# Performance work log

Hardware: AMD Instinct MI355X
Metric: run time of the kernel (lower is better)

Reference implementation:

```python
import math
import jax, jax.numpy as jnp
import numpy as np

B, T, C = 2, 2048, 1024
N_HEAD, N_KV_HEAD = 16, 4
HEAD_DIM = C // N_HEAD  # 64

def _rope(x, cos, sin):
    # x: (B, T, H, D); cos/sin: (1, T, 1, D//2)
    d = x.shape[3] // 2
    x1, x2 = x[..., :d], x[..., d:]
    return jnp.concatenate([x1 * cos + x2 * sin, -x1 * sin + x2 * cos], axis=3)

def _rms_norm(x):
    return x * jax.lax.rsqrt(jnp.mean(x * x, axis=-1, keepdims=True) + 1e-06)

def setup_inputs() -> dict:
    key = jax.random.key(0)
    ks = jax.random.split(key, 9)
    x = jax.random.normal(ks[0], (B, T, C), dtype=jnp.float32)
    ve = jax.random.normal(ks[1], (B, T, N_KV_HEAD * HEAD_DIM), dtype=jnp.float32)
    cos = jax.random.uniform(ks[2], (1, T, 1, HEAD_DIM // 2), dtype=jnp.float32)
    sin = jax.random.uniform(ks[3], (1, T, 1, HEAD_DIM // 2), dtype=jnp.float32)
    s = 1.0 / math.sqrt(C)
    Wq = jax.random.normal(ks[4], (C, N_HEAD * HEAD_DIM), dtype=jnp.float32) * s
    Wk = jax.random.normal(ks[5], (C, N_KV_HEAD * HEAD_DIM), dtype=jnp.float32) * s
    Wv = jax.random.normal(ks[6], (C, N_KV_HEAD * HEAD_DIM), dtype=jnp.float32) * s
    Wproj = jax.random.normal(ks[7], (C, C), dtype=jnp.float32) * s
    Wg = jax.random.normal(ks[8], (12, N_KV_HEAD), dtype=jnp.float32) * (1.0 / math.sqrt(12))
    return {"x": x, "ve": ve, "cos": cos, "sin": sin,
            "Wq": Wq, "Wk": Wk, "Wv": Wv, "Wproj": Wproj, "Wg": Wg,
            "window_size": 1024}

def reference(x, ve, cos, sin, Wq, Wk, Wv, Wproj, Wg, window_size):
    Bb, Tt, Cc = x.shape
    q = (x @ Wq).reshape(Bb, Tt, N_HEAD, HEAD_DIM)
    k = (x @ Wk).reshape(Bb, Tt, N_KV_HEAD, HEAD_DIM)
    v = (x @ Wv).reshape(Bb, Tt, N_KV_HEAD, HEAD_DIM)
    # value-embedding gate (has_ve layer)
    vee = ve.reshape(Bb, Tt, N_KV_HEAD, HEAD_DIM)
    gate = 3.0 * jax.nn.sigmoid(x[..., :12] @ Wg)  # (B, T, n_kv_head)
    v = v + gate[..., None] * vee
    q = _rope(q, cos, sin)
    k = _rope(k, cos, sin)
    q = _rms_norm(q) * 1.2
    k = _rms_norm(k) * 1.2
    repeats = N_HEAD // N_KV_HEAD
    k = jnp.repeat(k, repeats, axis=2)
    v = jnp.repeat(v, repeats, axis=2)
    # sliding-window causal mask
    row = jnp.arange(Tt)[:, None]
    col = jnp.arange(Tt)[None, :]
    mask = (row >= col) & (row - col <= window_size)
    bias = jnp.where(mask, 0.0, -1e9)  # (T, T)
    scale = 1.0 / math.sqrt(HEAD_DIM)
    scores = jnp.einsum("bqhd,bkhd->bhqk", q, k) * scale + bias[None, None]
    attn = jax.nn.softmax(scores, axis=-1)
    y = jnp.einsum("bhqk,bkhd->bqhd", attn, v).reshape(Bb, Tt, Cc)
    return y @ Wproj
```

## Files before the change

### kernel.cpp

```cpp
#include <hip/hip_runtime.h>


typedef __bf16 bf16x8 __attribute__((ext_vector_type(8)));
typedef __bf16 bf16x4 __attribute__((ext_vector_type(4)));
typedef float  f32x4  __attribute__((ext_vector_type(4)));

__device__ __forceinline__ void g2l16(const __bf16* gp, __bf16* lp) {
  __builtin_amdgcn_global_load_lds(
      (const __attribute__((address_space(1))) unsigned int*)(const void*)gp,
      (__attribute__((address_space(3))) unsigned int*)(void*)lp, 16, 0, 0);
}

__global__ void convert_gate(const float* __restrict__ in, __bf16* __restrict__ out,
                             float* __restrict__ gate, const float* __restrict__ Wg) {
  int i = (blockIdx.x * blockDim.x + threadIdx.x) * 8;
  float4 a = *(const float4*)(in + i);
  float4 b = *(const float4*)(in + i + 4);
  bf16x8 o;
  o[0] = (__bf16)a.x; o[1] = (__bf16)a.y; o[2] = (__bf16)a.z; o[3] = (__bf16)a.w;
  o[4] = (__bf16)b.x; o[5] = (__bf16)b.y; o[6] = (__bf16)b.z; o[7] = (__bf16)b.w;
  *(bf16x8*)(out + i) = o;
  if (threadIdx.x < 8) {
    int row = blockIdx.x * 2 + (threadIdx.x >> 2);
    int kvh = threadIdx.x & 3;
    float dot = 0.f;
    for (int j = 0; j < 12; ++j) dot += in[(size_t)row * 1024 + j] * Wg[j * 4 + kvh];
    gate[row * 4 + kvh] = 3.f / (1.f + expf(-dot));
  }
}

__global__ void transpose_weights(const float* __restrict__ Wq, const float* __restrict__ Wk,
                                  const float* __restrict__ Wv, const float* __restrict__ Wp,
                                  __bf16* __restrict__ Wt, __bf16* __restrict__ Wpt) {
  __shared__ float tile[32][33];
  int z = blockIdx.z;
  const float* in; __bf16* out; int Cc;
  if (z == 0)      { in = Wq; out = Wt;                 Cc = 1024; }
  else if (z == 1) { in = Wk; out = Wt + 1024 * 1024;   Cc = 256; }
  else if (z == 2) { in = Wv; out = Wt + 1280 * 1024;   Cc = 256; }
  else             { in = Wp; out = Wpt;                Cc = 1024; }
  const int R = 1024;
  int c0 = blockIdx.x * 32, r0 = blockIdx.y * 32;
  if (c0 >= Cc) return;
  int tx = threadIdx.x & 31, ty = threadIdx.x >> 5;
  for (int i = ty; i < 32; i += 8) tile[i][tx] = in[(size_t)(r0 + i) * Cc + c0 + tx];
  __syncthreads();
  for (int i = ty; i < 32; i += 8) out[(size_t)(c0 + i) * R + r0 + tx] = (__bf16)tile[tx][i];
}

__global__ __launch_bounds__(256) void gemm_qkv(const __bf16* __restrict__ A,
                                                const __bf16* __restrict__ Bt,
                                                const float* __restrict__ cosp,
                                                const float* __restrict__ sinp,
                                                const float* __restrict__ gate,
                                                const float* __restrict__ ve,
                                                __bf16* __restrict__ Qb,
                                                __bf16* __restrict__ Kb,
                                                __bf16* __restrict__ Vt) {
  const int K = 1024;
  __shared__ __bf16 As[128 * 32];
  __shared__ __bf16 Bs[128 * 32];
  int tid = threadIdx.x;
  int m0 = blockIdx.y * 128, n0 = blockIdx.x * 128;
  int w = tid >> 6, lane = tid & 63, quad = lane >> 4, l16 = lane & 15;
  int wm = (w >> 1) * 64, wn = (w & 1) * 64;

  f32x4 zero = {0.f, 0.f, 0.f, 0.f};
  f32x4 acc[4][4];
  for (int i = 0; i < 4; ++i) for (int j = 0; j < 4; ++j) acc[i][j] = zero;

  int ch0 = w * 2, ch1 = w * 2 + 1;
  int rsub = lane >> 2, cc = (lane & 3) * 8;
  const __bf16* gA0 = A + (size_t)(m0 + ch0 * 16 + rsub) * K + cc;
  const __bf16* gA1 = A + (size_t)(m0 + ch1 * 16 + rsub) * K + cc;
  const __bf16* gB0 = Bt + (size_t)(n0 + ch0 * 16 + rsub) * K + cc;
  const __bf16* gB1 = Bt + (size_t)(n0 + ch1 * 16 + rsub) * K + cc;
  __bf16* lA0 = &As[ch0 * 512]; __bf16* lA1 = &As[ch1 * 512];
  __bf16* lB0 = &Bs[ch0 * 512]; __bf16* lB1 = &Bs[ch1 * 512];

  for (int k0 = 0; k0 < K; k0 += 32) {
    __syncthreads();
    g2l16(gA0 + k0, lA0);
    g2l16(gA1 + k0, lA1);
    g2l16(gB0 + k0, lB0);
    g2l16(gB1 + k0, lB1);
    __syncthreads();
    bf16x8 af[4], bfr[4];
    for (int i = 0; i < 4; ++i) {
      af[i]  = *(const bf16x8*)(&As[(wm + i * 16 + l16) * 32 + quad * 8]);
      bfr[i] = *(const bf16x8*)(&Bs[(wn + i * 16 + l16) * 32 + quad * 8]);
    }
    for (int i = 0; i < 4; ++i)
      for (int j = 0; j < 4; ++j)
        acc[i][j] = __builtin_amdgcn_mfma_f32_16x16x32_bf16(af[i], bfr[j], acc[i][j], 0, 0, 0);
  }

  int ncol = n0 + wn;
  if (ncol < 1280) {
    __bf16* dstbase;
    if (ncol < 1024) dstbase = Qb + (size_t)(ncol >> 6) * 2048 * 64;
    else             dstbase = Kb + (size_t)((ncol - 1024) >> 6) * 2048 * 64;
    int nheads = (ncol < 1024) ? 16 : 4;
    for (int i = 0; i < 4; ++i) {
      for (int r = 0; r < 4; ++r) {
        int m = m0 + wm + i * 16 + quad * 4 + r;
        int bb = m >> 11, t = m & 2047;
        float c0 = cosp[t * 32 + l16], c1 = cosp[t * 32 + 16 + l16];
        float s0 = sinp[t * 32 + l16], s1 = sinp[t * 32 + 16 + l16];
        float v0 = acc[i][0][r], v1 = acc[i][1][r], v2 = acc[i][2][r], v3 = acc[i][3][r];
        float r0 = v0 * c0 + v2 * s0;
        float r1 = v1 * c1 + v3 * s1;
        float r2 = v2 * c0 - v0 * s0;
        float r3 = v3 * c1 - v1 * s1;
        float ss = r0 * r0 + r1 * r1 + r2 * r2 + r3 * r3;
        ss += __shfl_xor(ss, 1, 64); ss += __shfl_xor(ss, 2, 64);
        ss += __shfl_xor(ss, 4, 64); ss += __shfl_xor(ss, 8, 64);
        float sc = rsqrtf(ss * (1.f / 64.f) + 1e-6f) * 1.2f;
        __bf16* dst = dstbase + ((size_t)bb * nheads * 2048 + t) * 64;
        dst[l16]      = (__bf16)(r0 * sc);
        dst[16 + l16] = (__bf16)(r1 * sc);
        dst[32 + l16] = (__bf16)(r2 * sc);
        dst[48 + l16] = (__bf16)(r3 * sc);
      }
    }
  } else {
    int kvh = (ncol - 1280) >> 6;
    for (int i = 0; i < 4; ++i) {
      int mbase = m0 + wm + i * 16 + quad * 4;
      int bb = mbase >> 11;
      int t0 = mbase & 2047;
      float g4[4];
      for (int r = 0; r < 4; ++r) g4[r] = gate[(mbase + r) * 4 + kvh];
      for (int j = 0; j < 4; ++j) {
        int d = j * 16 + l16;
        bf16x4 pk;
        for (int r = 0; r < 4; ++r)
          pk[r] = (__bf16)(acc[i][j][r] + g4[r] * ve[(size_t)(mbase + r) * 256 + kvh * 64 + d]);
        *(bf16x4*)(Vt + ((size_t)(bb * 4 + kvh) * 64 + d) * 2048 + t0) = pk;
      }
    }
  }
}

__global__ __launch_bounds__(512) void attn_kernel(
    const __bf16* __restrict__ Q, const __bf16* __restrict__ K,
    const __bf16* __restrict__ Vt, __bf16* __restrict__ Y,
    const int* __restrict__ winp) {
  const int T = 2048, D = 64, NH = 16, NKV = 4;
  int b = blockIdx.z, h = blockIdx.y;
  int qb = (15 - blockIdx.x) * 128;
  int kvh = h >> 2;
  int tid = threadIdx.x, w = tid >> 6, lane = tid & 63, quad = lane >> 4, l16 = lane & 15;
  int window = *winp;
  int qw = qb + w * 16;

  __shared__ __bf16 Ks[64 * 72];
  __shared__ __bf16 Vs[64 * 72];
  __shared__ __bf16 Ps[8 * 16 * 72];

  const __bf16* Qbase = Q + ((size_t)(b * NH + h)) * T * D;
  bf16x8 qf0 = *(const bf16x8*)(Qbase + (size_t)(qw + l16) * D + quad * 8);
  bf16x8 qf1 = *(const bf16x8*)(Qbase + (size_t)(qw + l16) * D + quad * 8 + 32);

  const __bf16* Kbase = K  + ((size_t)(b * NKV + kvh)) * T * D;
  const __bf16* Vbase = Vt + ((size_t)(b * NKV + kvh)) * D * T;

  float lsum[4] = {0.f, 0.f, 0.f, 0.f};
  f32x4 zero = {0.f, 0.f, 0.f, 0.f};
  f32x4 o[4] = {zero, zero, zero, zero};

  int kstart = qb - window; if (kstart < 0) kstart = 0; kstart &= ~63;
  int kend = qb + 128;
  const float c1 = 0.125f * 1.44269504f;
  const float c2 = 12.0f * 1.44269504f;

  int sr = tid >> 3, sc8 = (tid & 7) * 8;
  bf16x8 kr = *(const bf16x8*)(Kbase + (size_t)(kstart + sr) * D + sc8);
  bf16x8 vr = *(const bf16x8*)(Vbase + (size_t)sr * T + kstart + sc8);

  for (int kt = kstart; kt < kend; kt += 64) {
    __syncthreads();
    *(bf16x8*)(&Ks[sr * 72 + sc8]) = kr;
    *(bf16x8*)(&Vs[sr * 72 + sc8]) = vr;
    __syncthreads();
    int ktn = kt + 64;
    if (ktn < kend) {
      kr = *(const bf16x8*)(Kbase + (size_t)(ktn + sr) * D + sc8);
      vr = *(const bf16x8*)(Vbase + (size_t)sr * T + ktn + sc8);
    }
    if (kt > qw + 15 || kt + 63 < qw - window) continue;

    f32x4 s[4];
    for (int kg = 0; kg < 4; ++kg) {
      bf16x8 k0 = *(const bf16x8*)(&Ks[(kg * 16 + l16) * 72 + quad * 8]);
      bf16x8 k1 = *(const bf16x8*)(&Ks[(kg * 16 + l16) * 72 + quad * 8 + 32]);
      s[kg] = __builtin_amdgcn_mfma_f32_16x16x32_bf16(qf0, k0, zero, 0, 0, 0);
      s[kg] = __builtin_amdgcn_mfma_f32_16x16x32_bf16(qf1, k1, s[kg], 0, 0, 0);
    }
    for (int r = 0; r < 4; ++r) {
      int q = qw + quad * 4 + r;
      for (int kg = 0; kg < 4; ++kg) {
        int ki = kt + kg * 16 + l16;
        bool ok = (ki <= q) && (q - ki <= window);
        float p = ok ? exp2f(s[kg][r] * c1 - c2) : 0.f;
        lsum[r] += p;
        Ps[w * 1152 + (quad * 4 + r) * 72 + kg * 16 + l16] = (__bf16)p;
      }
    }
    for (int koff = 0; koff < 64; koff += 32) {
      bf16x8 pf = *(const bf16x8*)(&Ps[w * 1152 + l16 * 72 + koff + quad * 8]);
      for (int j = 0; j < 4; ++j) {
        bf16x8 vf = *(const bf16x8*)(&Vs[(j * 16 + l16) * 72 + koff + quad * 8]);
        o[j] = __builtin_amdgcn_mfma_f32_16x16x32_bf16(pf, vf, o[j], 0, 0, 0);
      }
    }
  }

  for (int r = 0; r < 4; ++r) {
    float l = lsum[r];
    for (int off = 1; off < 16; off <<= 1) l += __shfl_xor(l, off, 64);
    float inv = 1.f / l;
    size_t base = ((size_t)(b * T + qw + quad * 4 + r)) * 1024 + h * 64 + l16;
    Y[base +  0] = (__bf16)(o[0][r] * inv);
    Y[base + 16] = (__bf16)(o[1][r] * inv);
    Y[base + 32] = (__bf16)(o[2][r] * inv);
    Y[base + 48] = (__bf16)(o[3][r] * inv);
  }
}

__global__ __launch_bounds__(256) void gemm_bt(const __bf16* __restrict__ A,
                                               const __bf16* __restrict__ Bt,
                                               float* __restrict__ C,
                                               int M, int N, int K) {
  __shared__ __bf16 As[128 * 32];
  __shared__ __bf16 Bs[128 * 32];
  int tid = threadIdx.x;
  int m0 = blockIdx.y * 128, n0 = blockIdx.x * 128;
  int w = tid >> 6, lane = tid & 63, quad = lane >> 4, l16 = lane & 15;
  int wm = (w >> 1) * 64, wn = (w & 1) * 64;

  f32x4 zero = {0.f, 0.f, 0.f, 0.f};
  f32x4 acc[4][4];
  for (int i = 0; i < 4; ++i) for (int j = 0; j < 4; ++j) acc[i][j] = zero;

  int ch0 = w * 2, ch1 = w * 2 + 1;
  int rsub = lane >> 2, cc = (lane & 3) * 8;
  const __bf16* gA0 = A + (size_t)(m0 + ch0 * 16 + rsub) * K + cc;
  const __bf16* gA1 = A + (size_t)(m0 + ch1 * 16 + rsub) * K + cc;
  const __bf16* gB0 = Bt + (size_t)(n0 + ch0 * 16 + rsub) * K + cc;
  const __bf16* gB1 = Bt + (size_t)(n0 + ch1 * 16 + rsub) * K + cc;
  __bf16* lA0 = &As[ch0 * 512]; __bf16* lA1 = &As[ch1 * 512];
  __bf16* lB0 = &Bs[ch0 * 512]; __bf16* lB1 = &Bs[ch1 * 512];

  for (int k0 = 0; k0 < K; k0 += 32) {
    __syncthreads();
    g2l16(gA0 + k0, lA0);
    g2l16(gA1 + k0, lA1);
    g2l16(gB0 + k0, lB0);
    g2l16(gB1 + k0, lB1);
    __syncthreads();
    bf16x8 af[4], bfr[4];
    for (int i = 0; i < 4; ++i) {
      af[i]  = *(const bf16x8*)(&As[(wm + i * 16 + l16) * 32 + quad * 8]);
      bfr[i] = *(const bf16x8*)(&Bs[(wn + i * 16 + l16) * 32 + quad * 8]);
    }
    for (int i = 0; i < 4; ++i)
      for (int j = 0; j < 4; ++j)
        acc[i][j] = __builtin_amdgcn_mfma_f32_16x16x32_bf16(af[i], bfr[j], acc[i][j], 0, 0, 0);
  }
  for (int i = 0; i < 4; ++i)
    for (int j = 0; j < 4; ++j)
      for (int r = 0; r < 4; ++r)
        C[(size_t)(m0 + wm + i * 16 + quad * 4 + r) * N + n0 + wn + j * 16 + l16] = acc[i][j][r];
}

extern "C" void kernel_launch(void* const* d_in, const int* in_sizes, int n_in,
                              void* d_out, int out_size, void* d_ws, size_t ws_size,
                              hipStream_t stream) {
  const float* x     = (const float*)d_in[0];
  const float* ve    = (const float*)d_in[1];
  const float* cosp  = (const float*)d_in[2];
  const float* sinp  = (const float*)d_in[3];
  const float* Wq    = (const float*)d_in[4];
  const float* Wk    = (const float*)d_in[5];
  const float* Wv    = (const float*)d_in[6];
  const float* Wproj = (const float*)d_in[7];
  const float* Wg    = (const float*)d_in[8];
  const int*   win   = (const int*)d_in[9];
  float* out = (float*)d_out;

  char* ws = (char*)d_ws;
  __bf16* xb   = (__bf16*)(ws);
  __bf16* Wt   = (__bf16*)(ws + 8388608);
  __bf16* Wpt  = (__bf16*)(ws + 11534336);
  float*  gate = (float*)(ws + 13631488);
  __bf16* Qb   = (__bf16*)(ws + 13697024);
  __bf16* Kb   = (__bf16*)(ws + 22085632);
  __bf16* Vt   = (__bf16*)(ws + 24182784);
  __bf16* Y    = (__bf16*)(ws + 26279936);

  convert_gate<<<2048, 256, 0, stream>>>(x, xb, gate, Wg);
  transpose_weights<<<dim3(32, 32, 4), 256, 0, stream>>>(Wq, Wk, Wv, Wproj, Wt, Wpt);
  gemm_qkv<<<dim3(12, 32), 256, 0, stream>>>(xb, Wt, cosp, sinp, gate, ve, Qb, Kb, Vt);
  attn_kernel<<<dim3(16, 16, 2), 512, 0, stream>>>(Qb, Kb, Vt, Y, win);
  gemm_bt<<<dim3(8, 32), 256, 0, stream>>>(Y, Wpt, out, 4096, 1024, 1024);
}
```

Before: 198.5 us.

## Merge prep kernels, halve GEMM M-tiles, restructure attention to direct global K/V loads

```diff
diff --git a/kernel.cpp b/kernel.cpp
--- a/kernel.cpp
+++ b/kernel.cpp
@@ -11,41 +11,44 @@
       (__attribute__((address_space(3))) unsigned int*)(void*)lp, 16, 0, 0);
 }
 
-__global__ void convert_gate(const float* __restrict__ in, __bf16* __restrict__ out,
-                             float* __restrict__ gate, const float* __restrict__ Wg) {
-  int i = (blockIdx.x * blockDim.x + threadIdx.x) * 8;
-  float4 a = *(const float4*)(in + i);
-  float4 b = *(const float4*)(in + i + 4);
-  bf16x8 o;
-  o[0] = (__bf16)a.x; o[1] = (__bf16)a.y; o[2] = (__bf16)a.z; o[3] = (__bf16)a.w;
-  o[4] = (__bf16)b.x; o[5] = (__bf16)b.y; o[6] = (__bf16)b.z; o[7] = (__bf16)b.w;
-  *(bf16x8*)(out + i) = o;
-  if (threadIdx.x < 8) {
-    int row = blockIdx.x * 2 + (threadIdx.x >> 2);
-    int kvh = threadIdx.x & 3;
-    float dot = 0.f;
-    for (int j = 0; j < 12; ++j) dot += in[(size_t)row * 1024 + j] * Wg[j * 4 + kvh];
-    gate[row * 4 + kvh] = 3.f / (1.f + expf(-dot));
-  }
-}
-
-__global__ void transpose_weights(const float* __restrict__ Wq, const float* __restrict__ Wk,
-                                  const float* __restrict__ Wv, const float* __restrict__ Wp,
-                                  __bf16* __restrict__ Wt, __bf16* __restrict__ Wpt) {
+__global__ void prep(const float* __restrict__ x, __bf16* __restrict__ xb,
+                     float* __restrict__ gate, const float* __restrict__ Wg,
+                     const float* __restrict__ Wq, const float* __restrict__ Wk,
+                     const float* __restrict__ Wv, const float* __restrict__ Wp,
+                     __bf16* __restrict__ Wt, __bf16* __restrict__ Wpt) {
   __shared__ float tile[32][33];
-  int z = blockIdx.z;
+  int bid = blockIdx.x;
+  if (bid < 2048) {
+    int i = (bid * 256 + threadIdx.x) * 8;
+    float4 a = *(const float4*)(x + i);
+    float4 b = *(const float4*)(x + i + 4);
+    bf16x8 o;
+    o[0] = (__bf16)a.x; o[1] = (__bf16)a.y; o[2] = (__bf16)a.z; o[3] = (__bf16)a.w;
+    o[4] = (__bf16)b.x; o[5] = (__bf16)b.y; o[6] = (__bf16)b.z; o[7] = (__bf16)b.w;
+    *(bf16x8*)(xb + i) = o;
+    if (threadIdx.x < 8) {
+      int row = bid * 2 + (threadIdx.x >> 2);
+      int kvh = threadIdx.x & 3;
+      float dot = 0.f;
+      for (int j = 0; j < 12; ++j) dot += x[(size_t)row * 1024 + j] * Wg[j * 4 + kvh];
+      gate[row * 4 + kvh] = 3.f / (1.f + expf(-dot));
+    }
+    return;
+  }
+  bid -= 2048;
+  int z = bid >> 10, r = bid & 1023;
+  int bx = r & 31, by = r >> 5;
   const float* in; __bf16* out; int Cc;
-  if (z == 0)      { in = Wq; out = Wt;                 Cc = 1024; }
-  else if (z == 1) { in = Wk; out = Wt + 1024 * 1024;   Cc = 256; }
-  else if (z == 2) { in = Wv; out = Wt + 1280 * 1024;   Cc = 256; }
-  else             { in = Wp; out = Wpt;                Cc = 1024; }
-  const int R = 1024;
-  int c0 = blockIdx.x * 32, r0 = blockIdx.y * 32;
+  if (z == 0)      { in = Wq; out = Wt;               Cc = 1024; }
+  else if (z == 1) { in = Wk; out = Wt + 1024 * 1024; Cc = 256; }
+  else if (z == 2) { in = Wv; out = Wt + 1280 * 1024; Cc = 256; }
+  else             { in = Wp; out = Wpt;              Cc = 1024; }
+  int c0 = bx * 32, r0 = by * 32;
   if (c0 >= Cc) return;
   int tx = threadIdx.x & 31, ty = threadIdx.x >> 5;
   for (int i = ty; i < 32; i += 8) tile[i][tx] = in[(size_t)(r0 + i) * Cc + c0 + tx];
   __syncthreads();
-  for (int i = ty; i < 32; i += 8) out[(size_t)(c0 + i) * R + r0 + tx] = (__bf16)tile[tx][i];
+  for (int i = ty; i < 32; i += 8) out[(size_t)(c0 + i) * 1024 + r0 + tx] = (__bf16)tile[tx][i];
 }
 
 __global__ __launch_bounds__(256) void gemm_qkv(const __bf16* __restrict__ A,
@@ -58,39 +61,37 @@
                                                 __bf16* __restrict__ Kb,
                                                 __bf16* __restrict__ Vt) {
   const int K = 1024;
-  __shared__ __bf16 As[128 * 32];
+  __shared__ __bf16 As[64 * 32];
   __shared__ __bf16 Bs[128 * 32];
   int tid = threadIdx.x;
-  int m0 = blockIdx.y * 128, n0 = blockIdx.x * 128;
+  int m0 = blockIdx.y * 64, n0 = blockIdx.x * 128;
   int w = tid >> 6, lane = tid & 63, quad = lane >> 4, l16 = lane & 15;
-  int wm = (w >> 1) * 64, wn = (w & 1) * 64;
+  int wm = (w >> 1) * 32, wn = (w & 1) * 64;
 
   f32x4 zero = {0.f, 0.f, 0.f, 0.f};
-  f32x4 acc[4][4];
-  for (int i = 0; i < 4; ++i) for (int j = 0; j < 4; ++j) acc[i][j] = zero;
-
-  int ch0 = w * 2, ch1 = w * 2 + 1;
+  f32x4 acc[2][4];
+  for (int i = 0; i < 2; ++i) for (int j = 0; j < 4; ++j) acc[i][j] = zero;
+
   int rsub = lane >> 2, cc = (lane & 3) * 8;
-  const __bf16* gA0 = A + (size_t)(m0 + ch0 * 16 + rsub) * K + cc;
-  const __bf16* gA1 = A + (size_t)(m0 + ch1 * 16 + rsub) * K + cc;
-  const __bf16* gB0 = Bt + (size_t)(n0 + ch0 * 16 + rsub) * K + cc;
-  const __bf16* gB1 = Bt + (size_t)(n0 + ch1 * 16 + rsub) * K + cc;
-  __bf16* lA0 = &As[ch0 * 512]; __bf16* lA1 = &As[ch1 * 512];
-  __bf16* lB0 = &Bs[ch0 * 512]; __bf16* lB1 = &Bs[ch1 * 512];
+  const __bf16* gA  = A  + (size_t)(m0 + w * 16 + rsub) * K + cc;
+  const __bf16* gB0 = Bt + (size_t)(n0 + (2 * w) * 16 + rsub) * K + cc;
+  const __bf16* gB1 = Bt + (size_t)(n0 + (2 * w + 1) * 16 + rsub) * K + cc;
+  __bf16* lA  = &As[w * 512];
+  __bf16* lB0 = &Bs[(2 * w) * 512];
+  __bf16* lB1 = &Bs[(2 * w + 1) * 512];
 
   for (int k0 = 0; k0 < K; k0 += 32) {
     __syncthreads();
-    g2l16(gA0 + k0, lA0);
-    g2l16(gA1 + k0, lA1);
+    g2l16(gA + k0, lA);
     g2l16(gB0 + k0, lB0);
     g2l16(gB1 + k0, lB1);
     __syncthreads();
-    bf16x8 af[4], bfr[4];
-    for (int i = 0; i < 4; ++i) {
-      af[i]  = *(const bf16x8*)(&As[(wm + i * 16 + l16) * 32 + quad * 8]);
-      bfr[i] = *(const bf16x8*)(&Bs[(wn + i * 16 + l16) * 32 + quad * 8]);
-    }
-    for (int i = 0; i < 4; ++i)
+    bf16x8 af[2], bfr[4];
+    for (int i = 0; i < 2; ++i)
+      af[i] = *(const bf16x8*)(&As[(wm + i * 16 + l16) * 32 + quad * 8]);
+    for (int j = 0; j < 4; ++j)
+      bfr[j] = *(const bf16x8*)(&Bs[(wn + j * 16 + l16) * 32 + quad * 8]);
+    for (int i = 0; i < 2; ++i)
       for (int j = 0; j < 4; ++j)
         acc[i][j] = __builtin_amdgcn_mfma_f32_16x16x32_bf16(af[i], bfr[j], acc[i][j], 0, 0, 0);
   }
@@ -101,7 +102,7 @@
     if (ncol < 1024) dstbase = Qb + (size_t)(ncol >> 6) * 2048 * 64;
     else             dstbase = Kb + (size_t)((ncol - 1024) >> 6) * 2048 * 64;
     int nheads = (ncol < 1024) ? 16 : 4;
-    for (int i = 0; i < 4; ++i) {
+    for (int i = 0; i < 2; ++i) {
       for (int r = 0; r < 4; ++r) {
         int m = m0 + wm + i * 16 + quad * 4 + r;
         int bb = m >> 11, t = m & 2047;
@@ -125,7 +126,7 @@
     }
   } else {
     int kvh = (ncol - 1280) >> 6;
-    for (int i = 0; i < 4; ++i) {
+    for (int i = 0; i < 2; ++i) {
       int mbase = m0 + wm + i * 16 + quad * 4;
       int bb = mbase >> 11;
       int t0 = mbase & 2047;
@@ -142,21 +143,19 @@
   }
 }
 
-__global__ __launch_bounds__(512) void attn_kernel(
+__global__ __launch_bounds__(256) void attn_kernel(
     const __bf16* __restrict__ Q, const __bf16* __restrict__ K,
     const __bf16* __restrict__ Vt, __bf16* __restrict__ Y,
     const int* __restrict__ winp) {
   const int T = 2048, D = 64, NH = 16, NKV = 4;
   int b = blockIdx.z, h = blockIdx.y;
-  int qb = (15 - blockIdx.x) * 128;
+  int qb = (31 - blockIdx.x) * 64;
   int kvh = h >> 2;
   int tid = threadIdx.x, w = tid >> 6, lane = tid & 63, quad = lane >> 4, l16 = lane & 15;
   int window = *winp;
   int qw = qb + w * 16;
 
-  __shared__ __bf16 Ks[64 * 72];
-  __shared__ __bf16 Vs[64 * 72];
-  __shared__ __bf16 Ps[8 * 16 * 72];
+  __shared__ __bf16 Ps[4 * 16 * 72];
 
   const __bf16* Qbase = Q + ((size_t)(b * NH + h)) * T * D;
   bf16x8 qf0 = *(const bf16x8*)(Qbase + (size_t)(qw + l16) * D + quad * 8);
@@ -169,50 +168,54 @@
   f32x4 zero = {0.f, 0.f, 0.f, 0.f};
   f32x4 o[4] = {zero, zero, zero, zero};
 
-  int kstart = qb - window; if (kstart < 0) kstart = 0; kstart &= ~63;
-  int kend = qb + 128;
+  int kw = qw - window;
+  int kt0 = (kw > 0) ? (kw & ~63) : 0;
+  int ktlast = (qw + 15) & ~63;
   const float c1 = 0.125f * 1.44269504f;
   const float c2 = 12.0f * 1.44269504f;
 
-  int sr = tid >> 3, sc8 = (tid & 7) * 8;
-  bf16x8 kr = *(const bf16x8*)(Kbase + (size_t)(kstart + sr) * D + sc8);
-  bf16x8 vr = *(const bf16x8*)(Vbase + (size_t)sr * T + kstart + sc8);
-
-  for (int kt = kstart; kt < kend; kt += 64) {
-    __syncthreads();
-    *(bf16x8*)(&Ks[sr * 72 + sc8]) = kr;
-    *(bf16x8*)(&Vs[sr * 72 + sc8]) = vr;
-    __syncthreads();
-    int ktn = kt + 64;
-    if (ktn < kend) {
-      kr = *(const bf16x8*)(Kbase + (size_t)(ktn + sr) * D + sc8);
-      vr = *(const bf16x8*)(Vbase + (size_t)sr * T + ktn + sc8);
-    }
-    if (kt > qw + 15 || kt + 63 < qw - window) continue;
-
+  for (int kt = kt0; kt <= ktlast; kt += 64) {
+    bf16x8 kf0[4], kf1[4];
+    for (int kg = 0; kg < 4; ++kg) {
+      const __bf16* gK = Kbase + (size_t)(kt + kg * 16 + l16) * D + quad * 8;
+      kf0[kg] = *(const bf16x8*)(gK);
+      kf1[kg] = *(const bf16x8*)(gK + 32);
+    }
+    bf16x8 vf[2][4];
+    for (int j = 0; j < 4; ++j) {
+      const __bf16* gV = Vbase + (size_t)(j * 16 + l16) * T + kt + quad * 8;
+      vf[0][j] = *(const bf16x8*)(gV);
+      vf[1][j] = *(const bf16x8*)(gV + 32);
+    }
     f32x4 s[4];
     for (int kg = 0; kg < 4; ++kg) {
-      bf16x8 k0 = *(const bf16x8*)(&Ks[(kg * 16 + l16) * 72 + quad * 8]);
-      bf16x8 k1 = *(const bf16x8*)(&Ks[(kg * 16 + l16) * 72 + quad * 8 + 32]);
-      s[kg] = __builtin_amdgcn_mfma_f32_16x16x32_bf16(qf0, k0, zero, 0, 0, 0);
-      s[kg] = __builtin_amdgcn_mfma_f32_16x16x32_bf16(qf1, k1, s[kg], 0, 0, 0);
-    }
-    for (int r = 0; r < 4; ++r) {
-      int q = qw + quad * 4 + r;
-      for (int kg = 0; kg < 4; ++kg) {
-        int ki = kt + kg * 16 + l16;
-        bool ok = (ki <= q) && (q - ki <= window);
-        float p = ok ? exp2f(s[kg][r] * c1 - c2) : 0.f;
-        lsum[r] += p;
-        Ps[w * 1152 + (quad * 4 + r) * 72 + kg * 16 + l16] = (__bf16)p;
+      s[kg] = __builtin_amdgcn_mfma_f32_16x16x32_bf16(qf0, kf0[kg], zero, 0, 0, 0);
+      s[kg] = __builtin_amdgcn_mfma_f32_16x16x32_bf16(qf1, kf1[kg], s[kg], 0, 0, 0);
+    }
+    bool clean = (kt + 63 <= qw) && (qw + 15 - kt <= window);
+    if (clean) {
+      for (int r = 0; r < 4; ++r)
+        for (int kg = 0; kg < 4; ++kg) {
+          float p = __builtin_amdgcn_exp2f(s[kg][r] * c1 - c2);
+          lsum[r] += p;
+          Ps[w * 1152 + (quad * 4 + r) * 72 + kg * 16 + l16] = (__bf16)p;
+        }
+    } else {
+      for (int r = 0; r < 4; ++r) {
+        int q = qw + quad * 4 + r;
+        for (int kg = 0; kg < 4; ++kg) {
+          int ki = kt + kg * 16 + l16;
+          bool ok = (ki <= q) && (q - ki <= window);
+          float p = ok ? __builtin_amdgcn_exp2f(s[kg][r] * c1 - c2) : 0.f;
+          lsum[r] += p;
+          Ps[w * 1152 + (quad * 4 + r) * 72 + kg * 16 + l16] = (__bf16)p;
+        }
       }
     }
-    for (int koff = 0; koff < 64; koff += 32) {
-      bf16x8 pf = *(const bf16x8*)(&Ps[w * 1152 + l16 * 72 + koff + quad * 8]);
-      for (int j = 0; j < 4; ++j) {
-        bf16x8 vf = *(const bf16x8*)(&Vs[(j * 16 + l16) * 72 + koff + quad * 8]);
-        o[j] = __builtin_amdgcn_mfma_f32_16x16x32_bf16(pf, vf, o[j], 0, 0, 0);
-      }
+    for (int koff = 0; koff < 2; ++koff) {
+      bf16x8 pf = *(const bf16x8*)(&Ps[w * 1152 + l16 * 72 + koff * 32 + quad * 8]);
+      for (int j = 0; j < 4; ++j)
+        o[j] = __builtin_amdgcn_mfma_f32_16x16x32_bf16(pf, vf[koff][j], o[j], 0, 0, 0);
     }
   }
 
@@ -228,47 +231,45 @@
   }
 }
 
-__global__ __launch_bounds__(256) void gemm_bt(const __bf16* __restrict__ A,
-                                               const __bf16* __restrict__ Bt,
-                                               float* __restrict__ C,
-                                               int M, int N, int K) {
-  __shared__ __bf16 As[128 * 32];
+__global__ __launch_bounds__(256) void gemm_proj(const __bf16* __restrict__ A,
+                                                 const __bf16* __restrict__ Bt,
+                                                 float* __restrict__ C,
+                                                 int M, int N, int K) {
+  __shared__ __bf16 As[64 * 32];
   __shared__ __bf16 Bs[128 * 32];
   int tid = threadIdx.x;
-  int m0 = blockIdx.y * 128, n0 = blockIdx.x * 128;
+  int m0 = blockIdx.y * 64, n0 = blockIdx.x * 128;
   int w = tid >> 6, lane = tid & 63, quad = lane >> 4, l16 = lane & 15;
-  int wm = (w >> 1) * 64, wn = (w & 1) * 64;
+  int wm = (w >> 1) * 32, wn = (w & 1) * 64;
 
   f32x4 zero = {0.f, 0.f, 0.f, 0.f};
-  f32x4 acc[4][4];
-  for (int i = 0; i < 4; ++i) for (int j = 0; j < 4; ++j) acc[i][j] = zero;
-
-  int ch0 = w * 2, ch1 = w * 2 + 1;
+  f32x4 acc[2][4];
+  for (int i = 0; i < 2; ++i) for (int j = 0; j < 4; ++j) acc[i][j] = zero;
+
   int rsub = lane >> 2, cc = (lane & 3) * 8;
-  const __bf16* gA0 = A + (size_t)(m0 + ch0 * 16 + rsub) * K + cc;
-  const __bf16* gA1 = A + (size_t)(m0 + ch1 * 16 + rsub) * K + cc;
-  const __bf16* gB0 = Bt + (size_t)(n0 + ch0 * 16 + rsub) * K + cc;
-  const __bf16* gB1 = Bt + (size_t)(n0 + ch1 * 16 + rsub) * K + cc;
-  __bf16* lA0 = &As[ch0 * 512]; __bf16* lA1 = &As[ch1 * 512];
-  __bf16* lB0 = &Bs[ch0 * 512]; __bf16* lB1 = &Bs[ch1 * 512];
+  const __bf16* gA  = A  + (size_t)(m0 + w * 16 + rsub) * K + cc;
+  const __bf16* gB0 = Bt + (size_t)(n0 + (2 * w) * 16 + rsub) * K + cc;
+  const __bf16* gB1 = Bt + (size_t)(n0 + (2 * w + 1) * 16 + rsub) * K + cc;
+  __bf16* lA  = &As[w * 512];
+  __bf16* lB0 = &Bs[(2 * w) * 512];
+  __bf16* lB1 = &Bs[(2 * w + 1) * 512];
 
   for (int k0 = 0; k0 < K; k0 += 32) {
     __syncthreads();
-    g2l16(gA0 + k0, lA0);
-    g2l16(gA1 + k0, lA1);
+    g2l16(gA + k0, lA);
     g2l16(gB0 + k0, lB0);
     g2l16(gB1 + k0, lB1);
     __syncthreads();
-    bf16x8 af[4], bfr[4];
-    for (int i = 0; i < 4; ++i) {
-      af[i]  = *(const bf16x8*)(&As[(wm + i * 16 + l16) * 32 + quad * 8]);
-      bfr[i] = *(const bf16x8*)(&Bs[(wn + i * 16 + l16) * 32 + quad * 8]);
-    }
-    for (int i = 0; i < 4; ++i)
+    bf16x8 af[2], bfr[4];
+    for (int i = 0; i < 2; ++i)
+      af[i] = *(const bf16x8*)(&As[(wm + i * 16 + l16) * 32 + quad * 8]);
+    for (int j = 0; j < 4; ++j)
+      bfr[j] = *(const bf16x8*)(&Bs[(wn + j * 16 + l16) * 32 + quad * 8]);
+    for (int i = 0; i < 2; ++i)
       for (int j = 0; j < 4; ++j)
         acc[i][j] = __builtin_amdgcn_mfma_f32_16x16x32_bf16(af[i], bfr[j], acc[i][j], 0, 0, 0);
   }
-  for (int i = 0; i < 4; ++i)
+  for (int i = 0; i < 2; ++i)
     for (int j = 0; j < 4; ++j)
       for (int r = 0; r < 4; ++r)
         C[(size_t)(m0 + wm + i * 16 + quad * 4 + r) * N + n0 + wn + j * 16 + l16] = acc[i][j][r];
@@ -299,9 +300,8 @@
   __bf16* Vt   = (__bf16*)(ws + 24182784);
   __bf16* Y    = (__bf16*)(ws + 26279936);
 
-  convert_gate<<<2048, 256, 0, stream>>>(x, xb, gate, Wg);
-  transpose_weights<<<dim3(32, 32, 4), 256, 0, stream>>>(Wq, Wk, Wv, Wproj, Wt, Wpt);
-  gemm_qkv<<<dim3(12, 32), 256, 0, stream>>>(xb, Wt, cosp, sinp, gate, ve, Qb, Kb, Vt);
-  attn_kernel<<<dim3(16, 16, 2), 512, 0, stream>>>(Qb, Kb, Vt, Y, win);
-  gemm_bt<<<dim3(8, 32), 256, 0, stream>>>(Y, Wpt, out, 4096, 1024, 1024);
-}
+  prep<<<2048 + 4096, 256, 0, stream>>>(x, xb, gate, Wg, Wq, Wk, Wv, Wproj, Wt, Wpt);
+  gemm_qkv<<<dim3(12, 64), 256, 0, stream>>>(xb, Wt, cosp, sinp, gate, ve, Qb, Kb, Vt);
+  attn_kernel<<<dim3(32, 16, 2), 256, 0, stream>>>(Qb, Kb, Vt, Y, win);
+  gemm_proj<<<dim3(8, 64), 256, 0, stream>>>(Y, Wpt, out, 4096, 1024, 1024);
+}
```

After: 263.0 us. +32.4%, slower.

## Merge prep kernels, deepen GEMM K-tile, keep attention P in registers

Applied to the files above, without the earlier changes.

```diff
diff --git a/kernel.cpp b/kernel.cpp
--- a/kernel.cpp
+++ b/kernel.cpp
@@ -11,41 +11,44 @@
       (__attribute__((address_space(3))) unsigned int*)(void*)lp, 16, 0, 0);
 }
 
-__global__ void convert_gate(const float* __restrict__ in, __bf16* __restrict__ out,
-                             float* __restrict__ gate, const float* __restrict__ Wg) {
-  int i = (blockIdx.x * blockDim.x + threadIdx.x) * 8;
-  float4 a = *(const float4*)(in + i);
-  float4 b = *(const float4*)(in + i + 4);
-  bf16x8 o;
-  o[0] = (__bf16)a.x; o[1] = (__bf16)a.y; o[2] = (__bf16)a.z; o[3] = (__bf16)a.w;
-  o[4] = (__bf16)b.x; o[5] = (__bf16)b.y; o[6] = (__bf16)b.z; o[7] = (__bf16)b.w;
-  *(bf16x8*)(out + i) = o;
-  if (threadIdx.x < 8) {
-    int row = blockIdx.x * 2 + (threadIdx.x >> 2);
-    int kvh = threadIdx.x & 3;
-    float dot = 0.f;
-    for (int j = 0; j < 12; ++j) dot += in[(size_t)row * 1024 + j] * Wg[j * 4 + kvh];
-    gate[row * 4 + kvh] = 3.f / (1.f + expf(-dot));
-  }
-}
-
-__global__ void transpose_weights(const float* __restrict__ Wq, const float* __restrict__ Wk,
-                                  const float* __restrict__ Wv, const float* __restrict__ Wp,
-                                  __bf16* __restrict__ Wt, __bf16* __restrict__ Wpt) {
+__global__ void prep(const float* __restrict__ x, __bf16* __restrict__ xb,
+                     float* __restrict__ gate, const float* __restrict__ Wg,
+                     const float* __restrict__ Wq, const float* __restrict__ Wk,
+                     const float* __restrict__ Wv, const float* __restrict__ Wp,
+                     __bf16* __restrict__ Wt, __bf16* __restrict__ Wpt) {
   __shared__ float tile[32][33];
-  int z = blockIdx.z;
+  int bid = blockIdx.x;
+  if (bid < 2048) {
+    int i = (bid * 256 + threadIdx.x) * 8;
+    float4 a = *(const float4*)(x + i);
+    float4 b = *(const float4*)(x + i + 4);
+    bf16x8 o;
+    o[0] = (__bf16)a.x; o[1] = (__bf16)a.y; o[2] = (__bf16)a.z; o[3] = (__bf16)a.w;
+    o[4] = (__bf16)b.x; o[5] = (__bf16)b.y; o[6] = (__bf16)b.z; o[7] = (__bf16)b.w;
+    *(bf16x8*)(xb + i) = o;
+    if (threadIdx.x < 8) {
+      int row = bid * 2 + (threadIdx.x >> 2);
+      int kvh = threadIdx.x & 3;
+      float dot = 0.f;
+      for (int j = 0; j < 12; ++j) dot += x[(size_t)row * 1024 + j] * Wg[j * 4 + kvh];
+      gate[row * 4 + kvh] = 3.f / (1.f + expf(-dot));
+    }
+    return;
+  }
+  bid -= 2048;
+  int z = bid >> 10, r = bid & 1023;
+  int bx = r & 31, by = r >> 5;
   const float* in; __bf16* out; int Cc;
-  if (z == 0)      { in = Wq; out = Wt;                 Cc = 1024; }
-  else if (z == 1) { in = Wk; out = Wt + 1024 * 1024;   Cc = 256; }
-  else if (z == 2) { in = Wv; out = Wt + 1280 * 1024;   Cc = 256; }
-  else             { in = Wp; out = Wpt;                Cc = 1024; }
-  const int R = 1024;
-  int c0 = blockIdx.x * 32, r0 = blockIdx.y * 32;
+  if (z == 0)      { in = Wq; out = Wt;               Cc = 1024; }
+  else if (z == 1) { in = Wk; out = Wt + 1024 * 1024; Cc = 256; }
+  else if (z == 2) { in = Wv; out = Wt + 1280 * 1024; Cc = 256; }
+  else             { in = Wp; out = Wpt;              Cc = 1024; }
+  int c0 = bx * 32, r0 = by * 32;
   if (c0 >= Cc) return;
   int tx = threadIdx.x & 31, ty = threadIdx.x >> 5;
   for (int i = ty; i < 32; i += 8) tile[i][tx] = in[(size_t)(r0 + i) * Cc + c0 + tx];
   __syncthreads();
-  for (int i = ty; i < 32; i += 8) out[(size_t)(c0 + i) * R + r0 + tx] = (__bf16)tile[tx][i];
+  for (int i = ty; i < 32; i += 8) out[(size_t)(c0 + i) * 1024 + r0 + tx] = (__bf16)tile[tx][i];
 }
 
 __global__ __launch_bounds__(256) void gemm_qkv(const __bf16* __restrict__ A,
@@ -58,8 +61,8 @@
                                                 __bf16* __restrict__ Kb,
                                                 __bf16* __restrict__ Vt) {
   const int K = 1024;
-  __shared__ __bf16 As[128 * 32];
-  __shared__ __bf16 Bs[128 * 32];
+  __shared__ __bf16 As[128 * 64];
+  __shared__ __bf16 Bs[128 * 64];
   int tid = threadIdx.x;
   int m0 = blockIdx.y * 128, n0 = blockIdx.x * 128;
   int w = tid >> 6, lane = tid & 63, quad = lane >> 4, l16 = lane & 15;
@@ -69,30 +72,33 @@
   f32x4 acc[4][4];
   for (int i = 0; i < 4; ++i) for (int j = 0; j < 4; ++j) acc[i][j] = zero;
 
-  int ch0 = w * 2, ch1 = w * 2 + 1;
   int rsub = lane >> 2, cc = (lane & 3) * 8;
-  const __bf16* gA0 = A + (size_t)(m0 + ch0 * 16 + rsub) * K + cc;
-  const __bf16* gA1 = A + (size_t)(m0 + ch1 * 16 + rsub) * K + cc;
-  const __bf16* gB0 = Bt + (size_t)(n0 + ch0 * 16 + rsub) * K + cc;
-  const __bf16* gB1 = Bt + (size_t)(n0 + ch1 * 16 + rsub) * K + cc;
-  __bf16* lA0 = &As[ch0 * 512]; __bf16* lA1 = &As[ch1 * 512];
-  __bf16* lB0 = &Bs[ch0 * 512]; __bf16* lB1 = &Bs[ch1 * 512];
-
-  for (int k0 = 0; k0 < K; k0 += 32) {
-    __syncthreads();
-    g2l16(gA0 + k0, lA0);
-    g2l16(gA1 + k0, lA1);
-    g2l16(gB0 + k0, lB0);
-    g2l16(gB1 + k0, lB1);
-    __syncthreads();
-    bf16x8 af[4], bfr[4];
-    for (int i = 0; i < 4; ++i) {
-      af[i]  = *(const bf16x8*)(&As[(wm + i * 16 + l16) * 32 + quad * 8]);
-      bfr[i] = *(const bf16x8*)(&Bs[(wn + i * 16 + l16) * 32 + quad * 8]);
-    }
-    for (int i = 0; i < 4; ++i)
-      for (int j = 0; j < 4; ++j)
-        acc[i][j] = __builtin_amdgcn_mfma_f32_16x16x32_bf16(af[i], bfr[j], acc[i][j], 0, 0, 0);
+  const __bf16* gA0 = A  + (size_t)(m0 + (2 * w) * 16 + rsub) * K + cc;
+  const __bf16* gA1 = A  + (size_t)(m0 + (2 * w + 1) * 16 + rsub) * K + cc;
+  const __bf16* gB0 = Bt + (size_t)(n0 + (2 * w) * 16 + rsub) * K + cc;
+  const __bf16* gB1 = Bt + (size_t)(n0 + (2 * w + 1) * 16 + rsub) * K + cc;
+  __bf16* lA00 = &As[(2 * w) * 512];     __bf16* lA01 = &As[4096 + (2 * w) * 512];
+  __bf16* lA10 = &As[(2 * w + 1) * 512]; __bf16* lA11 = &As[4096 + (2 * w + 1) * 512];
+  __bf16* lB00 = &Bs[(2 * w) * 512];     __bf16* lB01 = &Bs[4096 + (2 * w) * 512];
+  __bf16* lB10 = &Bs[(2 * w + 1) * 512]; __bf16* lB11 = &Bs[4096 + (2 * w + 1) * 512];
+
+  for (int k0 = 0; k0 < K; k0 += 64) {
+    __syncthreads();
+    g2l16(gA0 + k0, lA00); g2l16(gA0 + k0 + 32, lA01);
+    g2l16(gA1 + k0, lA10); g2l16(gA1 + k0 + 32, lA11);
+    g2l16(gB0 + k0, lB00); g2l16(gB0 + k0 + 32, lB01);
+    g2l16(gB1 + k0, lB10); g2l16(gB1 + k0 + 32, lB11);
+    __syncthreads();
+    for (int ks = 0; ks < 2; ++ks) {
+      bf16x8 af[4], bfr[4];
+      for (int i = 0; i < 4; ++i) {
+        af[i]  = *(const bf16x8*)(&As[ks * 4096 + (wm + i * 16 + l16) * 32 + quad * 8]);
+        bfr[i] = *(const bf16x8*)(&Bs[ks * 4096 + (wn + i * 16 + l16) * 32 + quad * 8]);
+      }
+      for (int i = 0; i < 4; ++i)
+        for (int j = 0; j < 4; ++j)
+          acc[i][j] = __builtin_amdgcn_mfma_f32_16x16x32_bf16(af[i], bfr[j], acc[i][j], 0, 0, 0);
+    }
   }
 
   int ncol = n0 + wn;
@@ -156,7 +162,6 @@
 
   __shared__ __bf16 Ks[64 * 72];
   __shared__ __bf16 Vs[64 * 72];
-  __shared__ __bf16 Ps[8 * 16 * 72];
 
   const __bf16* Qbase = Q + ((size_t)(b * NH + h)) * T * D;
   bf16x8 qf0 = *(const bf16x8*)(Qbase + (size_t)(qw + l16) * D + quad * 8);
@@ -165,14 +170,16 @@
   const __bf16* Kbase = K  + ((size_t)(b * NKV + kvh)) * T * D;
   const __bf16* Vbase = Vt + ((size_t)(b * NKV + kvh)) * D * T;
 
-  float lsum[4] = {0.f, 0.f, 0.f, 0.f};
+  float lsum = 0.f;
   f32x4 zero = {0.f, 0.f, 0.f, 0.f};
   f32x4 o[4] = {zero, zero, zero, zero};
 
-  int kstart = qb - window; if (kstart < 0) kstart = 0; kstart &= ~63;
+  int kw = qb - window;
+  int kstart = (kw > 0) ? (kw & ~63) : 0;
   int kend = qb + 128;
   const float c1 = 0.125f * 1.44269504f;
   const float c2 = 12.0f * 1.44269504f;
+  int q = qw + l16;
 
   int sr = tid >> 3, sc8 = (tid & 7) * 8;
   bf16x8 kr = *(const bf16x8*)(Kbase + (size_t)(kstart + sr) * D + sc8);
@@ -189,51 +196,69 @@
       vr = *(const bf16x8*)(Vbase + (size_t)sr * T + ktn + sc8);
     }
     if (kt > qw + 15 || kt + 63 < qw - window) continue;
-
-    f32x4 s[4];
-    for (int kg = 0; kg < 4; ++kg) {
-      bf16x8 k0 = *(const bf16x8*)(&Ks[(kg * 16 + l16) * 72 + quad * 8]);
-      bf16x8 k1 = *(const bf16x8*)(&Ks[(kg * 16 + l16) * 72 + quad * 8 + 32]);
-      s[kg] = __builtin_amdgcn_mfma_f32_16x16x32_bf16(qf0, k0, zero, 0, 0, 0);
-      s[kg] = __builtin_amdgcn_mfma_f32_16x16x32_bf16(qf1, k1, s[kg], 0, 0, 0);
-    }
-    for (int r = 0; r < 4; ++r) {
-      int q = qw + quad * 4 + r;
-      for (int kg = 0; kg < 4; ++kg) {
-        int ki = kt + kg * 16 + l16;
-        bool ok = (ki <= q) && (q - ki <= window);
-        float p = ok ? exp2f(s[kg][r] * c1 - c2) : 0.f;
-        lsum[r] += p;
-        Ps[w * 1152 + (quad * 4 + r) * 72 + kg * 16 + l16] = (__bf16)p;
-      }
-    }
-    for (int koff = 0; koff < 64; koff += 32) {
-      bf16x8 pf = *(const bf16x8*)(&Ps[w * 1152 + l16 * 72 + koff + quad * 8]);
-      for (int j = 0; j < 4; ++j) {
-        bf16x8 vf = *(const bf16x8*)(&Vs[(j * 16 + l16) * 72 + koff + quad * 8]);
-        o[j] = __builtin_amdgcn_mfma_f32_16x16x32_bf16(pf, vf, o[j], 0, 0, 0);
-      }
-    }
-  }
-
-  for (int r = 0; r < 4; ++r) {
-    float l = lsum[r];
-    for (int off = 1; off < 16; off <<= 1) l += __shfl_xor(l, off, 64);
-    float inv = 1.f / l;
-    size_t base = ((size_t)(b * T + qw + quad * 4 + r)) * 1024 + h * 64 + l16;
-    Y[base +  0] = (__bf16)(o[0][r] * inv);
-    Y[base + 16] = (__bf16)(o[1][r] * inv);
-    Y[base + 32] = (__bf16)(o[2][r] * inv);
-    Y[base + 48] = (__bf16)(o[3][r] * inv);
-  }
-}
-
-__global__ __launch_bounds__(256) void gemm_bt(const __bf16* __restrict__ A,
-                                               const __bf16* __restrict__ Bt,
-                                               float* __restrict__ C,
-                                               int M, int N, int K) {
-  __shared__ __bf16 As[128 * 32];
-  __shared__ __bf16 Bs[128 * 32];
+    bool clean = (kt + 63 <= qw) && (qw + 15 - kt <= window);
+
+    for (int g = 0; g < 2; ++g) {
+      int kb = g * 32;
+      bf16x8 ka0 = *(const bf16x8*)(&Ks[(kb + l16) * 72 + quad * 8]);
+      bf16x8 ka1 = *(const bf16x8*)(&Ks[(kb + l16) * 72 + quad * 8 + 32]);
+      f32x4 sA = __builtin_amdgcn_mfma_f32_16x16x32_bf16(ka0, qf0, zero, 0, 0, 0);
+      sA       = __builtin_amdgcn_mfma_f32_16x16x32_bf16(ka1, qf1, sA, 0, 0, 0);
+      bf16x8 kb0 = *(const bf16x8*)(&Ks[(kb + 16 + l16) * 72 + quad * 8]);
+      bf16x8 kb1 = *(const bf16x8*)(&Ks[(kb + 16 + l16) * 72 + quad * 8 + 32]);
+      f32x4 sB = __builtin_amdgcn_mfma_f32_16x16x32_bf16(kb0, qf0, zero, 0, 0, 0);
+      sB       = __builtin_amdgcn_mfma_f32_16x16x32_bf16(kb1, qf1, sB, 0, 0, 0);
+
+      bf16x8 pf;
+      if (clean) {
+        for (int r = 0; r < 4; ++r) {
+          float pA = __builtin_amdgcn_exp2f(sA[r] * c1 - c2);
+          float pB = __builtin_amdgcn_exp2f(sB[r] * c1 - c2);
+          lsum += pA + pB;
+          pf[r] = (__bf16)pA; pf[4 + r] = (__bf16)pB;
+        }
+      } else {
+        for (int r = 0; r < 4; ++r) {
+          int kiA = kt + kb + quad * 4 + r;
+          int kiB = kiA + 16;
+          bool okA = (kiA <= q) && (q - kiA <= window);
+          bool okB = (kiB <= q) && (q - kiB <= window);
+          float pA = okA ? __builtin_amdgcn_exp2f(sA[r] * c1 - c2) : 0.f;
+          float pB = okB ? __builtin_amdgcn_exp2f(sB[r] * c1 - c2) : 0.f;
+          lsum += pA + pB;
+          pf[r] = (__bf16)pA; pf[4 + r] = (__bf16)pB;
+        }
+      }
+      for (int dc = 0; dc < 4; ++dc) {
+        bf16x4 va = *(const bf16x4*)(&Vs[(dc * 16 + l16) * 72 + kb + quad * 4]);
+        bf16x4 vb = *(const bf16x4*)(&Vs[(dc * 16 + l16) * 72 + kb + 16 + quad * 4]);
+        bf16x8 vf;
+        vf[0] = va[0]; vf[1] = va[1]; vf[2] = va[2]; vf[3] = va[3];
+        vf[4] = vb[0]; vf[5] = vb[1]; vf[6] = vb[2]; vf[7] = vb[3];
+        o[dc] = __builtin_amdgcn_mfma_f32_16x16x32_bf16(vf, pf, o[dc], 0, 0, 0);
+      }
+    }
+  }
+
+  float l = lsum;
+  l += __shfl_xor(l, 16, 64);
+  l += __shfl_xor(l, 32, 64);
+  float inv = 1.f / l;
+  size_t base = ((size_t)(b * T + q)) * 1024 + h * 64 + quad * 4;
+  for (int dc = 0; dc < 4; ++dc) {
+    bf16x4 pk;
+    pk[0] = (__bf16)(o[dc][0] * inv); pk[1] = (__bf16)(o[dc][1] * inv);
+    pk[2] = (__bf16)(o[dc][2] * inv); pk[3] = (__bf16)(o[dc][3] * inv);
+    *(bf16x4*)(Y + base + dc * 16) = pk;
+  }
+}
+
+__global__ __launch_bounds__(256) void gemm_proj(const __bf16* __restrict__ A,
+                                                 const __bf16* __restrict__ Bt,
+                                                 float* __restrict__ C,
+                                                 int M, int N, int K) {
+  __shared__ __bf16 As[128 * 64];
+  __shared__ __bf16 Bs[128 * 64];
   int tid = threadIdx.x;
   int m0 = blockIdx.y * 128, n0 = blockIdx.x * 128;
   int w = tid >> 6, lane = tid & 63, quad = lane >> 4, l16 = lane & 15;
@@ -243,30 +268,33 @@
   f32x4 acc[4][4];
   for (int i = 0; i < 4; ++i) for (int j = 0; j < 4; ++j) acc[i][j] = zero;
 
-  int ch0 = w * 2, ch1 = w * 2 + 1;
   int rsub = lane >> 2, cc = (lane & 3) * 8;
-  const __bf16* gA0 = A + (size_t)(m0 + ch0 * 16 + rsub) * K + cc;
-  const __bf16* gA1 = A + (size_t)(m0 + ch1 * 16 + rsub) * K + cc;
-  const __bf16* gB0 = Bt + (size_t)(n0 + ch0 * 16 + rsub) * K + cc;
-  const __bf16* gB1 = Bt + (size_t)(n0 + ch1 * 16 + rsub) * K + cc;
-  __bf16* lA0 = &As[ch0 * 512]; __bf16* lA1 = &As[ch1 * 512];
-  __bf16* lB0 = &Bs[ch0 * 512]; __bf16* lB1 = &Bs[ch1 * 512];
-
-  for (int k0 = 0; k0 < K; k0 += 32) {
-    __syncthreads();
-    g2l16(gA0 + k0, lA0);
-    g2l16(gA1 + k0, lA1);
-    g2l16(gB0 + k0, lB0);
-    g2l16(gB1 + k0, lB1);
-    __syncthreads();
-    bf16x8 af[4], bfr[4];
-    for (int i = 0; i < 4; ++i) {
-      af[i]  = *(const bf16x8*)(&As[(wm + i * 16 + l16) * 32 + quad * 8]);
-      bfr[i] = *(const bf16x8*)(&Bs[(wn + i * 16 + l16) * 32 + quad * 8]);
-    }
-    for (int i = 0; i < 4; ++i)
-      for (int j = 0; j < 4; ++j)
-        acc[i][j] = __builtin_amdgcn_mfma_f32_16x16x32_bf16(af[i], bfr[j], acc[i][j], 0, 0, 0);
+  const __bf16* gA0 = A  + (size_t)(m0 + (2 * w) * 16 + rsub) * K + cc;
+  const __bf16* gA1 = A  + (size_t)(m0 + (2 * w + 1) * 16 + rsub) * K + cc;
+  const __bf16* gB0 = Bt + (size_t)(n0 + (2 * w) * 16 + rsub) * K + cc;
+  const __bf16* gB1 = Bt + (size_t)(n0 + (2 * w + 1) * 16 + rsub) * K + cc;
+  __bf16* lA00 = &As[(2 * w) * 512];     __bf16* lA01 = &As[4096 + (2 * w) * 512];
+  __bf16* lA10 = &As[(2 * w + 1) * 512]; __bf16* lA11 = &As[4096 + (2 * w + 1) * 512];
+  __bf16* lB00 = &Bs[(2 * w) * 512];     __bf16* lB01 = &Bs[4096 + (2 * w) * 512];
+  __bf16* lB10 = &Bs[(2 * w + 1) * 512]; __bf16* lB11 = &Bs[4096 + (2 * w + 1) * 512];
+
+  for (int k0 = 0; k0 < K; k0 += 64) {
+    __syncthreads();
+    g2l16(gA0 + k0, lA00); g2l16(gA0 + k0 + 32, lA01);
+    g2l16(gA1 + k0, lA10); g2l16(gA1 + k0 + 32, lA11);
+    g2l16(gB0 + k0, lB00); g2l16(gB0 + k0 + 32, lB01);
+    g2l16(gB1 + k0, lB10); g2l16(gB1 + k0 + 32, lB11);
+    __syncthreads();
+    for (int ks = 0; ks < 2; ++ks) {
+      bf16x8 af[4], bfr[4];
+      for (int i = 0; i < 4; ++i) {
+        af[i]  = *(const bf16x8*)(&As[ks * 4096 + (wm + i * 16 + l16) * 32 + quad * 8]);
+        bfr[i] = *(const bf16x8*)(&Bs[ks * 4096 + (wn + i * 16 + l16) * 32 + quad * 8]);
+      }
+      for (int i = 0; i < 4; ++i)
+        for (int j = 0; j < 4; ++j)
+          acc[i][j] = __builtin_amdgcn_mfma_f32_16x16x32_bf16(af[i], bfr[j], acc[i][j], 0, 0, 0);
+    }
   }
   for (int i = 0; i < 4; ++i)
     for (int j = 0; j < 4; ++j)
@@ -299,9 +327,8 @@
   __bf16* Vt   = (__bf16*)(ws + 24182784);
   __bf16* Y    = (__bf16*)(ws + 26279936);
 
-  convert_gate<<<2048, 256, 0, stream>>>(x, xb, gate, Wg);
-  transpose_weights<<<dim3(32, 32, 4), 256, 0, stream>>>(Wq, Wk, Wv, Wproj, Wt, Wpt);
+  prep<<<2048 + 4096, 256, 0, stream>>>(x, xb, gate, Wg, Wq, Wk, Wv, Wproj, Wt, Wpt);
   gemm_qkv<<<dim3(12, 32), 256, 0, stream>>>(xb, Wt, cosp, sinp, gate, ve, Qb, Kb, Vt);
   attn_kernel<<<dim3(16, 16, 2), 512, 0, stream>>>(Qb, Kb, Vt, Y, win);
-  gemm_bt<<<dim3(8, 32), 256, 0, stream>>>(Y, Wpt, out, 4096, 1024, 1024);
-}
+  gemm_proj<<<dim3(8, 32), 256, 0, stream>>>(Y, Wpt, out, 4096, 1024, 1024);
+}
```

Measured after the change: 178.9 us. 9.9% less time.
